# Kernel optimization log

Hardware: AMD Instinct MI355X
Metric: run time of the kernel (lower is better)

## Reference

```python
import jax, jax.numpy as jnp
import numpy as np

N_NODES = 500000
N_EDGES = 4000000
K = 4  # TAGConv hops


def _gcn_norm(edge_index, edge_weight, num_nodes):
    # PyG gcn_norm with add_self_loops=False (TAGConv default)
    src, dst = edge_index[0], edge_index[1]
    deg = jax.ops.segment_sum(edge_weight, dst, num_segments=num_nodes)
    dinv = jnp.where(deg > 0, jax.lax.rsqrt(deg), 0.0)
    return dinv[src] * edge_weight * dinv[dst]


def _tag_conv(x, src, dst, norm, Ws, b, num_nodes):
    # out = sum_{k=0..K} x_k @ Ws[k] + b,  x_k = hat(A) x_{k-1}
    out = x @ Ws[0]
    h = x
    for k in range(1, K + 1):
        msg = norm[:, None] * h[src]                      # [E, C]
        h = jax.ops.segment_sum(msg, dst, num_segments=num_nodes)
        out = out + h @ Ws[k]
    return out + b


def setup_inputs() -> dict:
    key = jax.random.key(0)
    ks = jax.random.split(key, 8)
    x = jax.random.normal(ks[0], (N_NODES, 2), dtype=jnp.float32)
    edge_index = jax.random.randint(ks[1], (2, N_EDGES), 0, N_NODES, dtype=jnp.int64)
    edge_weight = jax.random.uniform(ks[2], (N_EDGES,), dtype=jnp.float32)
    W1 = jax.random.normal(ks[3], (K + 1, 2, 16), dtype=jnp.float32) * 0.4
    b1 = jax.random.normal(ks[4], (16,), dtype=jnp.float32) * 0.1
    W2 = jax.random.normal(ks[5], (K + 1, 16, 16), dtype=jnp.float32) * 0.15
    b2 = jax.random.normal(ks[6], (16,), dtype=jnp.float32) * 0.1
    Wend = jax.random.normal(ks[7], (16, 1), dtype=jnp.float32) * 0.25
    return {"x": x, "edge_index": edge_index, "edge_weight": edge_weight,
            "W1": W1, "b1": b1, "W2": W2, "b2": b2, "Wend": Wend}


def reference(x, edge_index, edge_weight, W1, b1, W2, b2, Wend):
    src, dst = edge_index[0], edge_index[1]
    norm = _gcn_norm(edge_index, edge_weight, N_NODES)
    h = _tag_conv(x, src, dst, norm, W1, b1, N_NODES)      # conv1: 2 -> 16
    # num_layers=3 -> one relu+conv2 iteration
    h = jax.nn.relu(h)
    h = _tag_conv(h, src, dst, norm, W2, b2, N_NODES)      # conv2: 16 -> 16
    h = jax.nn.relu(h)
    y = h @ Wend                                           # endLinear (no bias)
    return jax.nn.sigmoid(y)                               # [N, 1]
```

## Files before the change

### kernel.cpp

```cpp
#include <hip/hip_runtime.h>
#include <hip/hip_fp16.h>
#include <math.h>


#define TB 256
#define TBIN 512
#define BSHIFT 11
#define BW 2048
#define CAPB 17408
#define CAP 26624
#define BIN_CHUNK 8192
#define WQ 8191.0f

typedef _Float16 half8 __attribute__((ext_vector_type(8)));
typedef float floatx4 __attribute__((ext_vector_type(4)));

__global__ __launch_bounds__(TBIN) void bin_kernel(
        const int* __restrict__ src, const int* __restrict__ dst,
        const float* __restrict__ w, int* __restrict__ binCount,
        uint2* __restrict__ binBuf, int E, int NB) {
    __shared__ int bcnt[256];
    __shared__ int bbase[256];
    for (int i = threadIdx.x; i < 256; i += TBIN) bcnt[i] = 0;
    __syncthreads();

    int base = blockIdx.x * BIN_CHUNK;
    int d[16];
#pragma unroll
    for (int j = 0; j < 16; j++) {
        int e = base + threadIdx.x + j * TBIN;
        d[j] = (e < E) ? dst[e] : -1;
        if (d[j] >= 0) atomicAdd(&bcnt[d[j] >> BSHIFT], 1);
    }
    __syncthreads();
    for (int i = threadIdx.x; i < NB; i += TBIN) {
        int c = bcnt[i];
        bbase[i] = c ? atomicAdd(&binCount[i], c) : 0;
        bcnt[i] = 0;
    }
    __syncthreads();
#pragma unroll
    for (int j = 0; j < 16; j++) {
        if (d[j] >= 0) {
            int e = base + threadIdx.x + j * TBIN;
            int b = d[j] >> BSHIFT;
            int off = bbase[b] + atomicAdd(&bcnt[b], 1);
            if (off < CAPB) {
                binBuf[(size_t)b * CAPB + off] =
                    make_uint2((unsigned)src[e] | ((unsigned)(d[j] & (BW - 1)) << 19),
                               __float_as_uint(w[e]));
            }
        }
    }
}

__global__ void build_kernel(const int* __restrict__ binCount, const uint2* __restrict__ binBuf,
                             unsigned* __restrict__ payload, int* __restrict__ seg,
                             float* __restrict__ dinv2, float* __restrict__ rdinv,
                             const float* __restrict__ x, __half2* __restrict__ z0,
                             int N, int NB) {
    __shared__ int   cnt[BW];
    __shared__ float wsum[BW];
    __shared__ int   start[BW];
    __shared__ int   tmp[TB];
    int b = blockIdx.x;
    int nBase = b << BSHIFT;
    int nCount = min(BW, N - nBase);
    int m = min(binCount[b], CAPB);

    for (int i = threadIdx.x; i < BW; i += TB) { cnt[i] = 0; wsum[i] = 0.0f; }
    __syncthreads();

    const uint2* recs = binBuf + (size_t)b * CAPB;
    for (int i = threadIdx.x; i < m; i += TB) {
        uint2 r = recs[i];
        int ld = r.x >> 19;
        atomicAdd(&cnt[ld], 1);
        atomicAdd(&wsum[ld], __uint_as_float(r.y));
    }
    __syncthreads();

    int b8 = threadIdx.x * 8;
    int c[8], s = 0;
#pragma unroll
    for (int j = 0; j < 8; j++) { c[j] = (cnt[b8 + j] + 7) & ~7; s += c[j]; }
    tmp[threadIdx.x] = s;
    __syncthreads();
    for (int off = 1; off < TB; off <<= 1) {
        int t = (threadIdx.x >= off) ? tmp[threadIdx.x - off] : 0;
        __syncthreads();
        tmp[threadIdx.x] += t;
        __syncthreads();
    }
    int run = tmp[threadIdx.x] - s;
#pragma unroll
    for (int j = 0; j < 8; j++) { start[b8 + j] = run; run += c[j]; }
    __syncthreads();

    size_t pbase = (size_t)b * CAP;
    for (int i = threadIdx.x; i < nCount; i += TB) {
        int n = nBase + i;
        int cc = cnt[i];
        int st = start[i];
        int ng = (cc + 7) >> 3;
        if (st >= CAP) { ng = 0; }
        else if (st + 8 * ng > CAP) { ng = (CAP - st) >> 3; }
        seg[n] = (st >> 3) | (ng << 16);
        for (int j = cc; j < 8 * ng; j++) payload[pbase + st + j] = 0;
        float dsum = wsum[i];
        float di = (dsum > 0.0f) ? rsqrtf(dsum) : 0.0f;
        dinv2[n] = di * di;
        rdinv[n] = dsum * di;
        float2 xv = reinterpret_cast<const float2*>(x)[n];
        z0[n] = __float22half2_rn(make_float2(di * xv.x, di * xv.y));
    }
    __syncthreads();
    for (int i = threadIdx.x; i < BW; i += TB) cnt[i] = start[i];
    __syncthreads();
    for (int i = threadIdx.x; i < m; i += TB) {
        uint2 r = recs[i];
        int ld = r.x >> 19;
        int pos = atomicAdd(&cnt[ld], 1);
        unsigned q = (unsigned)__float2int_rn(__uint_as_float(r.y) * WQ);
        if (pos < CAP) payload[pbase + pos] = (r.x & 0x7FFFFu) | (q << 19);
    }
}


__device__ __forceinline__ void gacc2m(const unsigned* __restrict__ payload,
                                       const __half2* __restrict__ zin,
                                       int beg, int ng, float& ax, float& ay) {
    for (int g = 0; g < ng; g++, beg += 8) {
        uint4 r0 = *reinterpret_cast<const uint4*>(payload + beg);
        uint4 r1 = *reinterpret_cast<const uint4*>(payload + beg + 4);
        unsigned r[8] = {r0.x, r0.y, r0.z, r0.w, r1.x, r1.y, r1.z, r1.w};
        __half2 v[8];
#pragma unroll
        for (int j = 0; j < 8; j++) v[j] = zin[r[j] & 0x7FFFFu];
#pragma unroll
        for (int j = 0; j < 8; j++) {
            float wv = (float)(r[j] >> 19) * (1.0f / WQ);
            float2 f = __half22float2(v[j]);
            ax += wv * f.x;
            ay += wv * f.y;
        }
    }
}

__device__ __forceinline__ void gacc4(const unsigned* __restrict__ payload,
                                      const __half* __restrict__ ubase,
                                      int beg, int ng, float* __restrict__ h) {
    for (int g = 0; g < ng; g++, beg += 8) {
        uint4 r0 = *reinterpret_cast<const uint4*>(payload + beg);
        uint4 r1 = *reinterpret_cast<const uint4*>(payload + beg + 4);
        unsigned r[8] = {r0.x, r0.y, r0.z, r0.w, r1.x, r1.y, r1.z, r1.w};
        float2 a[8];
#pragma unroll
        for (int j = 0; j < 8; j++)
            a[j] = *reinterpret_cast<const float2*>(ubase + 16LL * (int)(r[j] & 0x7FFFFu));
#pragma unroll
        for (int j = 0; j < 8; j++) {
            float wv = (float)(r[j] >> 19) * (1.0f / WQ);
            const __half2* hp = reinterpret_cast<const __half2*>(&a[j]);
            float2 v0 = __half22float2(hp[0]);
            float2 v1 = __half22float2(hp[1]);
            h[0] += wv * v0.x;
            h[1] += wv * v0.y;
            h[2] += wv * v1.x;
            h[3] += wv * v1.y;
        }
    }
}


__global__ void hop2_kernel(const int* __restrict__ seg, const unsigned* __restrict__ payload,
                            const __half2* __restrict__ zin, const float* __restrict__ dinv2,
                            __half2* __restrict__ zout, int N) {
    int n = blockIdx.x * TB + threadIdx.x;
    if (n >= N) return;
    int sp = seg[n];
    int beg = (n >> BSHIFT) * CAP + ((sp & 0xFFFF) << 3);
    int ng = sp >> 16;
    float ax = 0.0f, ay = 0.0f;
    gacc2m(payload, zin, beg, ng, ax, ay);
    float sc = dinv2[n];
    zout[n] = __float22half2_rn(make_float2(ax * sc, ay * sc));
}

__global__ void hop2_final_kernel(const int* __restrict__ seg, const unsigned* __restrict__ payload,
                                  const __half2* __restrict__ zbuf,
                                  const float* __restrict__ x,
                                  const float* __restrict__ rdinv, const float* __restrict__ dinv2,
                                  const float* __restrict__ W1, const float* __restrict__ b1,
                                  __half* __restrict__ g0, __half* __restrict__ u0, int N) {
    __shared__ float Ws[160];
    __shared__ float bs[16];
    for (int i = threadIdx.x; i < 160; i += blockDim.x) Ws[i] = W1[i];
    if (threadIdx.x < 16) bs[threadIdx.x] = b1[threadIdx.x];
    __syncthreads();

    int n = blockIdx.x * TB + threadIdx.x;
    if (n >= N) return;

    int sp = seg[n];
    int beg = (n >> BSHIFT) * CAP + ((sp & 0xFFFF) << 3);
    int ng = sp >> 16;
    const __half2* z3 = zbuf + (size_t)3 * N;
    float ax = 0.0f, ay = 0.0f;
    gacc2m(payload, z3, beg, ng, ax, ay);
    float sc = dinv2[n];
    float rd = rdinv[n];

    float coeff[10];
    {
        float2 v = reinterpret_cast<const float2*>(x)[n];
        coeff[0] = v.x; coeff[1] = v.y;
    }
#pragma unroll
    for (int k = 1; k <= 3; k++) {
        float2 v = __half22float2(zbuf[(size_t)k * N + n]);
        coeff[2 * k + 0] = rd * v.x;
        coeff[2 * k + 1] = rd * v.y;
    }
    coeff[8] = rd * sc * ax;
    coeff[9] = rd * sc * ay;

    float o[16];
#pragma unroll
    for (int c = 0; c < 16; c++) o[c] = bs[c];
#pragma unroll
    for (int j = 0; j < 10; j++) {
        float cf = coeff[j];
#pragma unroll
        for (int c = 0; c < 16; c++) o[c] += cf * Ws[j * 16 + c];
    }
#pragma unroll
    for (int c = 0; c < 16; c++) o[c] = fmaxf(o[c], 0.0f);

    float di = sc * rd;

    __half2 gp[8], up[8];
#pragma unroll
    for (int q = 0; q < 8; q++) {
        gp[q] = __float22half2_rn(make_float2(o[2 * q], o[2 * q + 1]));
        up[q] = __float22half2_rn(make_float2(di * o[2 * q], di * o[2 * q + 1]));
    }
    float4* gw = reinterpret_cast<float4*>(g0 + 16LL * n);
    gw[0] = *reinterpret_cast<float4*>(&gp[0]);
    gw[1] = *reinterpret_cast<float4*>(&gp[4]);
    float4* uw = reinterpret_cast<float4*>(u0 + 16LL * n);
    uw[0] = *reinterpret_cast<float4*>(&up[0]);
    uw[1] = *reinterpret_cast<float4*>(&up[4]);
}

__global__ void hop16_kernel(const int* __restrict__ seg, const unsigned* __restrict__ payload,
                             const __half* __restrict__ uin, const float* __restrict__ dinv2,
                             __half* __restrict__ uout, int N) {
    int gid = blockIdx.x * TB + threadIdx.x;
    int n = gid >> 2, quarter = gid & 3;
    if (n >= N) return;
    int sp = seg[n];
    int beg = (n >> BSHIFT) * CAP + ((sp & 0xFFFF) << 3);
    int ng = sp >> 16;

    float h[4] = {0.0f, 0.0f, 0.0f, 0.0f};
    gacc4(payload, uin + 4 * quarter, beg, ng, h);

    float sc = dinv2[n];
    __half2 p[2];
    p[0] = __float22half2_rn(make_float2(h[0] * sc, h[1] * sc));
    p[1] = __float22half2_rn(make_float2(h[2] * sc, h[3] * sc));
    *reinterpret_cast<float2*>(uout + 16LL * n + 4 * quarter) = *reinterpret_cast<float2*>(&p[0]);
}

__global__ void hop16_final_kernel(const int* __restrict__ seg, const unsigned* __restrict__ payload,
                                   const __half* __restrict__ g0, const __half* __restrict__ ubuf,
                                   const float* __restrict__ rdinv, const float* __restrict__ dinv2,
                                   const float* __restrict__ W2, const float* __restrict__ b2,
                                   const float* __restrict__ Wend, float* __restrict__ out, int N) {
    int lane = threadIdx.x & 63;
    int wave = threadIdx.x >> 6;
    int q = lane >> 4;
    int nn = lane & 15;
    int node_base = (blockIdx.x * 4 + wave) * 16;
    int node = node_base + nn;
    int nodec = min(node, N - 1);

    half8 bf[3];
#pragma unroll
    for (int t = 0; t < 3; t++) {
        half8 bv;
#pragma unroll
        for (int i = 0; i < 8; i++) {
            int K = 32 * t + 8 * q + i;
            K = (K < 80) ? K : 79;
            bv[i] = (_Float16)W2[K * 16 + nn];
        }
        bf[t] = bv;
    }
    float bsv = b2[nn];
    float wev = Wend[nn];

    int sp = seg[nodec];
    int beg = (nodec >> BSHIFT) * CAP + ((sp & 0xFFFF) << 3);
    int ng = sp >> 16;
    const __half* u3 = ubuf + (size_t)3 * 16 * N;
    float h[4] = {0.0f, 0.0f, 0.0f, 0.0f};
    gacc4(payload, u3 + 4 * q, beg, ng, h);

    float rd = rdinv[nodec];
    float sc = dinv2[nodec];

    const __half* a0p = ((q < 2) ? g0 : (ubuf + (size_t)16 * N)) + 16LL * nodec + 8 * (q & 1);
    half8 a0 = *reinterpret_cast<const half8*>(a0p);
    a0 = a0 * ((q >= 2) ? (_Float16)rd : (_Float16)1.0f);

    const __half* a1p = ((q < 2) ? (ubuf + (size_t)2 * 16 * N) : (ubuf + (size_t)3 * 16 * N))
                        + 16LL * nodec + 8 * (q & 1);
    half8 a1 = *reinterpret_cast<const half8*>(a1p);
    a1 = a1 * (_Float16)rd;

    float s4 = rd * sc;
    __half2 hh0 = __floats2half2_rn(h[0] * s4, h[1] * s4);
    __half2 hh1 = __floats2half2_rn(h[2] * s4, h[3] * s4);
    int p0, p1;
    p0 = *reinterpret_cast<int*>(&hh0);
    p1 = *reinterpret_cast<int*>(&hh1);
    int srcA = (nn + (q << 5)) & 63;
    int srcB = (srcA + 16) & 63;
    int lo0 = __shfl(p0, srcA, 64);
    int lo1 = __shfl(p1, srcA, 64);
    int hi0 = __shfl(p0, srcB, 64);
    int hi1 = __shfl(p1, srcB, 64);
    if (q >= 2) { lo0 = 0; lo1 = 0; hi0 = 0; hi1 = 0; }
    union { half8 v; int u[4]; } a2;
    a2.u[0] = lo0; a2.u[1] = lo1; a2.u[2] = hi0; a2.u[3] = hi1;

    floatx4 acc = {bsv, bsv, bsv, bsv};
    acc = __builtin_amdgcn_mfma_f32_16x16x32_f16(a0, bf[0], acc, 0, 0, 0);
    acc = __builtin_amdgcn_mfma_f32_16x16x32_f16(a1, bf[1], acc, 0, 0, 0);
    acc = __builtin_amdgcn_mfma_f32_16x16x32_f16(a2.v, bf[2], acc, 0, 0, 0);

    float svals[4];
#pragma unroll
    for (int r = 0; r < 4; r++) {
        float o = fmaxf(acc[r], 0.0f) * wev;
        o += __shfl_xor(o, 1, 64);
        o += __shfl_xor(o, 2, 64);
        o += __shfl_xor(o, 4, 64);
        o += __shfl_xor(o, 8, 64);
        svals[r] = o;
    }
    if (nn == 0) {
#pragma unroll
        for (int r = 0; r < 4; r++) {
            int on = node_base + q * 4 + r;
            if (on < N) out[on] = 1.0f / (1.0f + __expf(-svals[r]));
        }
    }
}

extern "C" void kernel_launch(void* const* d_in, const int* in_sizes, int n_in,
                              void* d_out, int out_size, void* d_ws, size_t ws_size,
                              hipStream_t stream) {
    const float* x    = (const float*)d_in[0];
    const int*   ei   = (const int*)d_in[1];
    const float* w    = (const float*)d_in[2];
    const float* W1   = (const float*)d_in[3];
    const float* b1   = (const float*)d_in[4];
    const float* W2   = (const float*)d_in[5];
    const float* b2   = (const float*)d_in[6];
    const float* Wend = (const float*)d_in[7];
    float* out = (float*)d_out;

    const int N = in_sizes[0] / 2;
    const int E = in_sizes[2];
    const int NB = (N + BW - 1) / BW;

    const int* src = ei;
    const int* dst = ei + E;

    int*      binCount = (int*)d_ws;
    unsigned* payload  = (unsigned*)(binCount + 1024);
    int*      seg      = (int*)(payload + (size_t)NB * CAP);
    float*    dinv2    = (float*)(seg + N);
    float*    rdinv    = dinv2 + N;
    __half2*  zbuf     = (__half2*)(rdinv + N);
    __half*   g0       = (__half*)(zbuf + (size_t)4 * N);
    __half*   ubuf     = g0 + (size_t)16 * N;
    uint2*    binBuf   = (uint2*)(ubuf + (size_t)16 * N);

    const int gE_bin = (E + BIN_CHUNK - 1) / BIN_CHUNK;
    const int gN   = (N + TB - 1) / TB;
    const int gN4  = (4 * N + TB - 1) / TB;
    const int gFin = (N + 63) / 64;

    hipMemsetAsync(binCount, 0, 1024 * sizeof(int), stream);

    bin_kernel<<<gE_bin, TBIN, 0, stream>>>(src, dst, w, binCount, binBuf, E, NB);
    build_kernel<<<NB, TB, 0, stream>>>(binCount, binBuf, payload, seg, dinv2, rdinv, x, zbuf, N, NB);

    for (int k = 1; k <= 3; k++) {
        hop2_kernel<<<gN, TB, 0, stream>>>(seg, payload, zbuf + (size_t)(k - 1) * N,
                                           dinv2, zbuf + (size_t)k * N, N);
    }
    hop2_final_kernel<<<gN, TB, 0, stream>>>(seg, payload, zbuf, x, rdinv, dinv2,
                                             W1, b1, g0, ubuf, N);

    for (int k = 1; k <= 3; k++) {
        hop16_kernel<<<gN4, TB, 0, stream>>>(seg, payload, ubuf + (size_t)(k - 1) * 16 * N,
                                             dinv2, ubuf + (size_t)k * 16 * N, N);
    }
    hop16_final_kernel<<<gFin, TB, 0, stream>>>(seg, payload, g0, ubuf, rdinv, dinv2,
                                                W2, b2, Wend, out, N);
}
```

Before: 572.6 us.

## Scatter CSR payload in eight local-destination windows with larger build blocks

The build kernel now runs with 512 threads and fills the payload in eight passes, each handling only records whose local destination lies in a 256-node window. Padding zeros for that window are written in the same pass. The goal is to make global payload writes land in a compact region per pass, improving write locality and cache coalescing. The cost is re-reading the bin records eight times and adding more barriers and shared memory (an extra cursor array).

```diff
diff --git a/kernel.cpp b/kernel.cpp
--- a/kernel.cpp
+++ b/kernel.cpp
@@ -4,6 +4,7 @@
 
 
 #define TB 256
+#define TBLD 512
 #define TBIN 512
 #define BSHIFT 11
 #define BW 2048
@@ -54,25 +55,27 @@
     }
 }
 
-__global__ void build_kernel(const int* __restrict__ binCount, const uint2* __restrict__ binBuf,
-                             unsigned* __restrict__ payload, int* __restrict__ seg,
-                             float* __restrict__ dinv2, float* __restrict__ rdinv,
-                             const float* __restrict__ x, __half2* __restrict__ z0,
-                             int N, int NB) {
+__global__ __launch_bounds__(TBLD) void build_kernel(
+        const int* __restrict__ binCount, const uint2* __restrict__ binBuf,
+        unsigned* __restrict__ payload, int* __restrict__ seg,
+        float* __restrict__ dinv2, float* __restrict__ rdinv,
+        const float* __restrict__ x, __half2* __restrict__ z0,
+        int N, int NB) {
     __shared__ int   cnt[BW];
     __shared__ float wsum[BW];
     __shared__ int   start[BW];
-    __shared__ int   tmp[TB];
+    __shared__ int   cur[BW];
+    __shared__ int   tmp[TBLD];
     int b = blockIdx.x;
     int nBase = b << BSHIFT;
     int nCount = min(BW, N - nBase);
     int m = min(binCount[b], CAPB);
 
-    for (int i = threadIdx.x; i < BW; i += TB) { cnt[i] = 0; wsum[i] = 0.0f; }
+    for (int i = threadIdx.x; i < BW; i += TBLD) { cnt[i] = 0; wsum[i] = 0.0f; }
     __syncthreads();
 
     const uint2* recs = binBuf + (size_t)b * CAPB;
-    for (int i = threadIdx.x; i < m; i += TB) {
+    for (int i = threadIdx.x; i < m; i += TBLD) {
         uint2 r = recs[i];
         int ld = r.x >> 19;
         atomicAdd(&cnt[ld], 1);
@@ -80,13 +83,13 @@
     }
     __syncthreads();
 
-    int b8 = threadIdx.x * 8;
-    int c[8], s = 0;
-#pragma unroll
-    for (int j = 0; j < 8; j++) { c[j] = (cnt[b8 + j] + 7) & ~7; s += c[j]; }
+    int b4 = threadIdx.x * 4;
+    int c[4], s = 0;
+#pragma unroll
+    for (int j = 0; j < 4; j++) { c[j] = (cnt[b4 + j] + 7) & ~7; s += c[j]; }
     tmp[threadIdx.x] = s;
     __syncthreads();
-    for (int off = 1; off < TB; off <<= 1) {
+    for (int off = 1; off < TBLD; off <<= 1) {
         int t = (threadIdx.x >= off) ? tmp[threadIdx.x - off] : 0;
         __syncthreads();
         tmp[threadIdx.x] += t;
@@ -94,11 +97,12 @@
     }
     int run = tmp[threadIdx.x] - s;
 #pragma unroll
-    for (int j = 0; j < 8; j++) { start[b8 + j] = run; run += c[j]; }
+    for (int j = 0; j < 4; j++) { start[b4 + j] = run; run += c[j]; }
     __syncthreads();
 
     size_t pbase = (size_t)b * CAP;
-    for (int i = threadIdx.x; i < nCount; i += TB) {
+    for (int i = threadIdx.x; i < BW; i += TBLD) cur[i] = start[i];
+    for (int i = threadIdx.x; i < nCount; i += TBLD) {
         int n = nBase + i;
         int cc = cnt[i];
         int st = start[i];
@@ -106,7 +110,6 @@
         if (st >= CAP) { ng = 0; }
         else if (st + 8 * ng > CAP) { ng = (CAP - st) >> 3; }
         seg[n] = (st >> 3) | (ng << 16);
-        for (int j = cc; j < 8 * ng; j++) payload[pbase + st + j] = 0;
         float dsum = wsum[i];
         float di = (dsum > 0.0f) ? rsqrtf(dsum) : 0.0f;
         dinv2[n] = di * di;
@@ -115,14 +118,30 @@
         z0[n] = __float22half2_rn(make_float2(di * xv.x, di * xv.y));
     }
     __syncthreads();
-    for (int i = threadIdx.x; i < BW; i += TB) cnt[i] = start[i];
-    __syncthreads();
-    for (int i = threadIdx.x; i < m; i += TB) {
-        uint2 r = recs[i];
-        int ld = r.x >> 19;
-        int pos = atomicAdd(&cnt[ld], 1);
-        unsigned q = (unsigned)__float2int_rn(__uint_as_float(r.y) * WQ);
-        if (pos < CAP) payload[pbase + pos] = (r.x & 0x7FFFFu) | (q << 19);
+
+    for (int t = 0; t < 8; t++) {
+        int lo = t << 8, hi = lo + 256;
+        for (int i = threadIdx.x; i < m; i += TBLD) {
+            uint2 r = recs[i];
+            int ld = r.x >> 19;
+            if (ld >= lo && ld < hi) {
+                int pos = atomicAdd(&cur[ld], 1);
+                unsigned q = (unsigned)__float2int_rn(__uint_as_float(r.y) * WQ);
+                if (pos < CAP) payload[pbase + pos] = (r.x & 0x7FFFFu) | (q << 19);
+            }
+        }
+        if (threadIdx.x < 256) {
+            int i = lo + threadIdx.x;
+            if (i < nCount) {
+                int cc = cnt[i];
+                int st = start[i];
+                int ng = (cc + 7) >> 3;
+                if (st >= CAP) ng = 0;
+                else if (st + 8 * ng > CAP) ng = (CAP - st) >> 3;
+                for (int j = cc; j < 8 * ng; j++) payload[pbase + st + j] = 0;
+            }
+        }
+        __syncthreads();
     }
 }
 
@@ -398,7 +417,7 @@
     hipMemsetAsync(binCount, 0, 1024 * sizeof(int), stream);
 
     bin_kernel<<<gE_bin, TBIN, 0, stream>>>(src, dst, w, binCount, binBuf, E, NB);
-    build_kernel<<<NB, TB, 0, stream>>>(binCount, binBuf, payload, seg, dinv2, rdinv, x, zbuf, N, NB);
+    build_kernel<<<NB, TBLD, 0, stream>>>(binCount, binBuf, payload, seg, dinv2, rdinv, x, zbuf, N, NB);
 
     for (int k = 1; k <= 3; k++) {
         hop2_kernel<<<gN, TB, 0, stream>>>(seg, payload, zbuf + (size_t)(k - 1) * N,
```

New measurement: 674.3 us. +17.8%, slower.
